# Performance work log

Hardware: AMD Instinct MI355X
Metric: run time of the kernel (lower is better)

## Reference

```python
import jax, jax.numpy as jnp
import numpy as np

B, L, H = 2, 2048, 1024
NH, KVH = 16, 4
HD = H // NH          # 64
G = NH // KVH         # 4 query heads per kv head


def setup_inputs() -> dict:
    key = jax.random.key(0)
    ks = jax.random.split(key, 10)
    s = 0.02
    return {
        "hidden_states": jax.random.normal(ks[0], (B, L, H), dtype=jnp.float32),
        "attention_mask": jnp.zeros((B, 1, L, L), dtype=jnp.float32),
        "Wq": jax.random.normal(ks[1], (H, H), dtype=jnp.float32) * s,
        "bq": jnp.zeros((H,), dtype=jnp.float32),
        "Wk": jax.random.normal(ks[2], (KVH * HD, H), dtype=jnp.float32) * s,
        "bk": jnp.zeros((KVH * HD,), dtype=jnp.float32),
        "Wv": jax.random.normal(ks[3], (KVH * HD, H), dtype=jnp.float32) * s,
        "bv": jnp.zeros((KVH * HD,), dtype=jnp.float32),
        "Wo": jax.random.normal(ks[4], (H, H), dtype=jnp.float32) * s,
        "bo": jnp.zeros((H,), dtype=jnp.float32),
    }


def reference(hidden_states, attention_mask, Wq, bq, Wk, bk, Wv, bv, Wo, bo):
    x = hidden_states
    # projections (torch Linear: x @ W.T + b)
    q = (x @ Wq.T + bq).reshape(B, L, NH, HD).transpose(0, 2, 1, 3)   # [B,NH,L,HD]
    k = (x @ Wk.T + bk).reshape(B, L, KVH, HD).transpose(0, 2, 1, 3)  # [B,KVH,L,HD]
    v = (x @ Wv.T + bv).reshape(B, L, KVH, HD).transpose(0, 2, 1, 3)
    # GQA: group query heads per kv head instead of repeat_interleave (same math)
    qg = q.reshape(B, KVH, G, L, HD)
    scores = jnp.einsum("bkgqd,bkld->bkgql", qg, k) / jnp.sqrt(jnp.float32(HD))
    scores = scores + attention_mask[:, :, None, :, :]  # mask broadcasts over heads
    attn = jax.nn.softmax(scores, axis=-1)              # dropout p=0 -> identity
    ctx = jnp.einsum("bkgql,bkld->bkgqd", attn, v)      # [B,KVH,G,L,HD]
    ctx = ctx.reshape(B, NH, L, HD).transpose(0, 2, 1, 3).reshape(B, L, H)
    return ctx @ Wo.T + bo
```

## Files before the change

### kernel.cpp

```cpp
#include <hip/hip_runtime.h>

#define B_   2
#define L_   2048
#define H_   1024
#define NH_  16
#define KVH_ 4
#define HD_  64

typedef short short8 __attribute__((ext_vector_type(8)));
typedef float f32x4 __attribute__((ext_vector_type(4)));
typedef unsigned short u16x4 __attribute__((ext_vector_type(4)));
typedef unsigned int u32x2 __attribute__((ext_vector_type(2)));

#define LOG2E 1.4426950408889634f
#define QSC   0.18033688011112042f
#define MFMA  __builtin_amdgcn_mfma_f32_16x16x32_bf16

#if __has_builtin(__builtin_amdgcn_exp2f)
#define EXP2(x) __builtin_amdgcn_exp2f(x)
#else
#define EXP2(x) exp2f(x)
#endif

static __device__ __forceinline__ unsigned short f2bf(float f) {
  unsigned int u = __float_as_uint(f);
  u += 0x7FFFu + ((u >> 16) & 1u);
  return (unsigned short)(u >> 16);
}

static __device__ __forceinline__ unsigned int cvtpk(float lo, float hi) {
  unsigned int r;
  asm("v_cvt_pk_bf16_f32 %0, %1, %2" : "=v"(r) : "v"(lo), "v"(hi));
  return r;
}

static __device__ __forceinline__ void gload_lds16(const void* g, void* l) {
  __builtin_amdgcn_global_load_lds(
      (const __attribute__((address_space(1))) unsigned int*)g,
      (__attribute__((address_space(3))) unsigned int*)l, 16, 0, 0);
}

__global__ __launch_bounds__(256) void k_convert_x(const float* __restrict__ x,
                                                   unsigned short* __restrict__ xb) {
  size_t i = ((size_t)blockIdx.x * 256 + threadIdx.x) * 4;
  float4 v = *(const float4*)(x + i);
  u16x4 o = { f2bf(v.x), f2bf(v.y), f2bf(v.z), f2bf(v.w) };
  *(u16x4*)(xb + i) = o;
}

__global__ __launch_bounds__(256) void k_convert_w(const float* __restrict__ Wq,
                                                   const float* __restrict__ Wk,
                                                   const float* __restrict__ Wv,
                                                   const float* __restrict__ Wo,
                                                   unsigned short* __restrict__ wcat,
                                                   unsigned short* __restrict__ wo_b) {
  int r = blockIdx.x;
  int c = threadIdx.x * 4;
  const float* src;
  unsigned short* dst;
  if (r < 1024)      { src = Wq + (size_t)r * 1024;          dst = wcat + (size_t)r * 1024; }
  else if (r < 1280) { src = Wk + (size_t)(r - 1024) * 1024; dst = wcat + (size_t)r * 1024; }
  else if (r < 1536) { src = Wv + (size_t)(r - 1280) * 1024; dst = wcat + (size_t)r * 1024; }
  else               { src = Wo + (size_t)(r - 1536) * 1024; dst = wo_b + (size_t)(r - 1536) * 1024; }
  float4 v = *(const float4*)(src + c);
  u16x4 o = { f2bf(v.x), f2bf(v.y), f2bf(v.z), f2bf(v.w) };
  *(u16x4*)(dst + c) = o;
}

__global__ __launch_bounds__(256) void k_mask_scan(const float* __restrict__ mask,
                                                   unsigned char* __restrict__ flags) {
  const int blk = blockIdx.x;
  const int b = blk >> 10, qb = (blk >> 5) & 31, kb = blk & 31;
  const float* base = mask + ((size_t)b * L_ + qb * 64) * L_ + kb * 64;
  const int t = threadIdx.x;
  const int r0 = t >> 4, c = (t & 15) * 4;
  bool nz = false;
#pragma unroll
  for (int i = 0; i < 4; ++i) {
    float4 v = *(const float4*)(base + (size_t)(r0 + i * 16) * L_ + c);
    nz |= (v.x != 0.f) | (v.y != 0.f) | (v.z != 0.f) | (v.w != 0.f);
  }
  __shared__ int anyv;
  if (t == 0) anyv = 0;
  __syncthreads();
  if (__any(nz) && (t & 63) == 0) atomicOr(&anyv, 1);
  __syncthreads();
  if (t == 0) flags[blk] = (unsigned char)anyv;
}

template <int MODE>
__global__ __launch_bounds__(256) void k_gemm(const unsigned short* __restrict__ A,
                                              const unsigned short* __restrict__ Bt,
                                              const float* __restrict__ bias0,
                                              const float* __restrict__ bias1,
                                              const float* __restrict__ bias2,
                                              unsigned short* __restrict__ q_ws,
                                              unsigned short* __restrict__ k_ws,
                                              unsigned short* __restrict__ vt_ws,
                                              float* __restrict__ outp) {
  const int bn = blockIdx.x, bm = blockIdx.y;
  const int t = threadIdx.x;
  const int lane = t & 63, li = lane & 15, g = lane >> 4;
  const int wid = t >> 6, wr = wid >> 1, wc = wid & 1;
  __shared__ unsigned short lds_a[128 * 32];
  __shared__ unsigned short lds_b[128 * 32];

  const f32x4 z = {0.f, 0.f, 0.f, 0.f};
  f32x4 acc[4][4];
#pragma unroll
  for (int m = 0; m < 4; ++m)
#pragma unroll
    for (int n = 0; n < 4; ++n) acc[m][n] = z;

  const int c0 = t, c1 = 256 + t;
  const int r0 = c0 >> 2, o0 = (c0 & 3) * 8;
  const int r1 = c1 >> 2, o1 = (c1 & 3) * 8;
  const unsigned short* a0p = A + (size_t)(bm * 128 + r0) * 1024 + o0;
  const unsigned short* a1p = A + (size_t)(bm * 128 + r1) * 1024 + o1;
  const unsigned short* b0p = Bt + (size_t)(bn * 128 + r0) * 1024 + o0;
  const unsigned short* b1p = Bt + (size_t)(bn * 128 + r1) * 1024 + o1;

  for (int kt = 0; kt < 1024; kt += 32) {
    gload_lds16(a0p + kt, &lds_a[c0 * 8]);
    gload_lds16(a1p + kt, &lds_a[c1 * 8]);
    gload_lds16(b0p + kt, &lds_b[c0 * 8]);
    gload_lds16(b1p + kt, &lds_b[c1 * 8]);
    __syncthreads();
    short8 af[4], bf[4];
#pragma unroll
    for (int m = 0; m < 4; ++m) af[m] = *(const short8*)&lds_a[(wr * 64 + m * 16 + li) * 32 + g * 8];
#pragma unroll
    for (int n = 0; n < 4; ++n) bf[n] = *(const short8*)&lds_b[(wc * 64 + n * 16 + li) * 32 + g * 8];
#pragma unroll
    for (int m = 0; m < 4; ++m)
#pragma unroll
      for (int n = 0; n < 4; ++n)
        acc[m][n] = MFMA(af[m], bf[n], acc[m][n], 0, 0, 0);
    __syncthreads();
  }

#pragma unroll
  for (int m = 0; m < 4; ++m) {
    const int row0 = bm * 128 + wr * 64 + m * 16 + 4 * g;
#pragma unroll
    for (int n = 0; n < 4; ++n) {
      const int col = bn * 128 + wc * 64 + n * 16 + li;
      f32x4 v = acc[m][n];
      if (MODE == 1) {
        const float bias = bias0[col];
#pragma unroll
        for (int r = 0; r < 4; ++r) outp[(size_t)(row0 + r) * 1024 + col] = v[r] + bias;
      } else {
        if (col < 1024) {
          const float bias = bias0[col];
#pragma unroll
          for (int r = 0; r < 4; ++r) q_ws[(size_t)(row0 + r) * 1024 + col] = f2bf((v[r] + bias) * QSC);
        } else if (col < 1280) {
          const int cc = col - 1024;
          const float bias = bias1[cc];
#pragma unroll
          for (int r = 0; r < 4; ++r) k_ws[(size_t)(row0 + r) * 256 + cc] = f2bf(v[r] + bias);
        } else {
          const int cc = col - 1280;
          const float bias = bias2[cc];
          const int kvh = cc >> 6, d = cc & 63;
          const int b = row0 >> 11, l0 = row0 & 2047;
          u16x4 pk = { f2bf(v[0] + bias), f2bf(v[1] + bias), f2bf(v[2] + bias), f2bf(v[3] + bias) };
          *(u16x4*)(vt_ws + ((size_t)((b * KVH_ + kvh) * 64 + d)) * 2048 + l0) = pk;
        }
      }
    }
  }
}

__global__ __launch_bounds__(256, 2) void k_attn(const unsigned short* __restrict__ q_ws,
                                                 const unsigned short* __restrict__ k_ws,
                                                 const unsigned short* __restrict__ vt_ws,
                                                 const float* __restrict__ mask,
                                                 const unsigned char* __restrict__ mflags,
                                                 unsigned short* __restrict__ ctx) {
  const int bk = blockIdx.x;
  const int qt = blockIdx.y;
  const int b = bk >> 2, kvh = bk & 3;
  const int t = threadIdx.x;
  const int wid = t >> 6, lane = t & 63, li = lane & 15, g = lane >> 4;
  const int h = kvh * 4 + wid;

  __shared__ unsigned short lds_k[2][64 * 64];
  __shared__ unsigned short lds_v[2][64 * 64];
  __shared__ unsigned short lds_p[4][2][16 * 72];

  const unsigned short* qlane = q_ws + ((size_t)b * L_ + qt * 32 + li) * H_ + h * HD_ + g * 8;
  short8 qf[2][2];
#pragma unroll
  for (int qif = 0; qif < 2; ++qif)
#pragma unroll
    for (int hh = 0; hh < 2; ++hh)
      qf[qif][hh] = *(const short8*)(qlane + (size_t)qif * 16 * H_ + hh * 32);

  const unsigned int* fp = (const unsigned int*)(mflags + b * 1024 + (qt >> 1) * 32);
  unsigned int fm = 0;
#pragma unroll
  for (int w = 0; w < 8; ++w) {
    unsigned int wv = fp[w];
    fm |= ((wv & 0x000000FFu) ? 1u : 0u) << (w * 4 + 0);
    fm |= ((wv & 0x0000FF00u) ? 1u : 0u) << (w * 4 + 1);
    fm |= ((wv & 0x00FF0000u) ? 1u : 0u) << (w * 4 + 2);
    fm |= ((wv & 0xFF000000u) ? 1u : 0u) << (w * 4 + 3);
  }
  fm = __builtin_amdgcn_readfirstlane(fm);

  const int srow = t >> 3, sgr = t & 7;
  const int swz = (sgr ^ (srow & 7)) * 8;
  const unsigned short* ksrc = k_ws + ((size_t)b * L_ + srow) * 256 + kvh * 64 + swz;
  const unsigned short* vsrc = vt_ws + ((size_t)(b * KVH_ + kvh) * 64 + srow) * 2048 + swz;

  const f32x4 z = {0.f, 0.f, 0.f, 0.f};
  f32x4 o[2][4];
#pragma unroll
  for (int qif = 0; qif < 2; ++qif)
#pragma unroll
    for (int db = 0; db < 4; ++db) o[qif][db] = z;
  float l_run[2] = {0.f, 0.f};

  const int rsw = li & 7;

#define STAGE(buf, kt)                                                       \
  {                                                                          \
    _Pragma("unroll")                                                        \
    for (int i = 0; i < 2; ++i) {                                            \
      gload_lds16(ksrc + ((size_t)(kt) * 64 + i * 32) * 256,                 \
                  &lds_k[buf][(t + 256 * i) * 8]);                           \
      gload_lds16(vsrc + (size_t)i * 32 * 2048 + (kt) * 64,                  \
                  &lds_v[buf][(t + 256 * i) * 8]);                           \
    }                                                                        \
  }

  STAGE(0, 0);
  __syncthreads();

#pragma unroll 1
  for (int kt = 0; kt < 32; ++kt) {
    const int cur = kt & 1;
    if (kt + 1 < 32) STAGE(cur ^ 1, kt + 1);

    short8 kf[4][2], vf[4][2];
#pragma unroll
    for (int x = 0; x < 4; ++x) {
      const int row = (x * 16 + li) * 64;
      kf[x][0] = *(const short8*)&lds_k[cur][row + ((0 + g) ^ rsw) * 8];
      kf[x][1] = *(const short8*)&lds_k[cur][row + ((4 + g) ^ rsw) * 8];
      vf[x][0] = *(const short8*)&lds_v[cur][row + ((0 + g) ^ rsw) * 8];
      vf[x][1] = *(const short8*)&lds_v[cur][row + ((4 + g) ^ rsw) * 8];
    }

    f32x4 sv[2][4];
    __builtin_amdgcn_s_setprio(1);
#pragma unroll
    for (int qif = 0; qif < 2; ++qif)
#pragma unroll
      for (int kb = 0; kb < 4; ++kb) {
        sv[qif][kb] = MFMA(kf[kb][0], qf[qif][0], z, 0, 0, 0);
        sv[qif][kb] = MFMA(kf[kb][1], qf[qif][1], sv[qif][kb], 0, 0, 0);
      }
    __builtin_amdgcn_s_setprio(0);

    if (fm & (1u << kt)) {
#pragma unroll
      for (int qif = 0; qif < 2; ++qif) {
        const float* mrow = mask + ((size_t)b * L_ + qt * 32 + qif * 16 + li) * L_ + kt * 64 + 4 * g;
#pragma unroll
        for (int kb = 0; kb < 4; ++kb) {
          float4 mv = *(const float4*)(mrow + kb * 16);
          sv[qif][kb][0] = fmaf(mv.x, LOG2E, sv[qif][kb][0]);
          sv[qif][kb][1] = fmaf(mv.y, LOG2E, sv[qif][kb][1]);
          sv[qif][kb][2] = fmaf(mv.z, LOG2E, sv[qif][kb][2]);
          sv[qif][kb][3] = fmaf(mv.w, LOG2E, sv[qif][kb][3]);
        }
      }
    }

#pragma unroll
    for (int qif = 0; qif < 2; ++qif) {
      float ts = 0.f;
#pragma unroll
      for (int kb = 0; kb < 4; ++kb)
#pragma unroll
        for (int r = 0; r < 4; ++r) {
          const float p = EXP2(sv[qif][kb][r]);
          sv[qif][kb][r] = p;
          ts += p;
        }
      l_run[qif] += ts;
#pragma unroll
      for (int kb = 0; kb < 4; ++kb) {
        u32x2 pk = { cvtpk(sv[qif][kb][0], sv[qif][kb][1]),
                     cvtpk(sv[qif][kb][2], sv[qif][kb][3]) };
        *(u32x2*)&lds_p[wid][qif][li * 72 + kb * 16 + 4 * g] = pk;
      }
    }

    __builtin_amdgcn_s_setprio(1);
#pragma unroll
    for (int qif = 0; qif < 2; ++qif)
#pragma unroll
      for (int kjh = 0; kjh < 2; ++kjh) {
        short8 pb = *(const short8*)&lds_p[wid][qif][li * 72 + kjh * 32 + g * 8];
#pragma unroll
        for (int db = 0; db < 4; ++db)
          o[qif][db] = MFMA(vf[db][kjh], pb, o[qif][db], 0, 0, 0);
      }
    __builtin_amdgcn_s_setprio(0);

    __syncthreads();
  }
#undef STAGE

#pragma unroll
  for (int qif = 0; qif < 2; ++qif) {
    float lt = l_run[qif];
    lt += __shfl_xor(lt, 16);
    lt += __shfl_xor(lt, 32);
    const float inv = 1.0f / lt;
    unsigned short* cp = ctx + ((size_t)b * L_ + qt * 32 + qif * 16 + li) * H_ + h * HD_ + 4 * g;
#pragma unroll
    for (int db = 0; db < 4; ++db) {
      u32x2 pk = { cvtpk(o[qif][db][0] * inv, o[qif][db][1] * inv),
                   cvtpk(o[qif][db][2] * inv, o[qif][db][3] * inv) };
      *(u32x2*)(cp + db * 16) = pk;
    }
  }
}

extern "C" void kernel_launch(void* const* d_in, const int* in_sizes, int n_in,
                              void* d_out, int out_size, void* d_ws, size_t ws_size,
                              hipStream_t stream) {
  const float* x    = (const float*)d_in[0];
  const float* mask = (const float*)d_in[1];
  const float* Wq   = (const float*)d_in[2];
  const float* bq   = (const float*)d_in[3];
  const float* Wk   = (const float*)d_in[4];
  const float* bk   = (const float*)d_in[5];
  const float* Wv   = (const float*)d_in[6];
  const float* bv   = (const float*)d_in[7];
  const float* Wo   = (const float*)d_in[8];
  const float* bo   = (const float*)d_in[9];
  float* out = (float*)d_out;

  char* ws = (char*)d_ws;
  unsigned short* xb    = (unsigned short*)(ws);
  unsigned short* ctx   = xb;
  unsigned short* wcat  = (unsigned short*)(ws + 8388608);
  unsigned short* wo_b  = (unsigned short*)(ws + 11534336);
  unsigned short* q_ws  = (unsigned short*)(ws + 13631488);
  unsigned short* k_ws  = (unsigned short*)(ws + 22020096);
  unsigned short* vt_ws = (unsigned short*)(ws + 24117248);
  unsigned char*  mflg  = (unsigned char*)(ws + 26214400);

  k_convert_x<<<dim3(4096), dim3(256), 0, stream>>>(x, xb);
  k_convert_w<<<dim3(2560), dim3(256), 0, stream>>>(Wq, Wk, Wv, Wo, wcat, wo_b);
  k_mask_scan<<<dim3(2048), dim3(256), 0, stream>>>(mask, mflg);
  k_gemm<0><<<dim3(12, 32), dim3(256), 0, stream>>>(xb, wcat, bq, bk, bv, q_ws, k_ws, vt_ws, nullptr);
  k_attn<<<dim3(8, 64), dim3(256), 0, stream>>>(q_ws, k_ws, vt_ws, mask, mflg, ctx);
  k_gemm<1><<<dim3(8, 32), dim3(256), 0, stream>>>(ctx, wo_b, bo, nullptr, nullptr,
                                                   nullptr, nullptr, nullptr, out);
}
```

Measured before the change: 122.0 us.

## Fuse prep kernels and triple-buffer K/V with K-fragment register prefetch

Merges the x conversion, weight conversion and mask scan into one launch, cutting two kernel launches. In attention, K/V LDS staging goes from double to triple buffering with a prefetch distance of two tiles. The next tile's K fragments are read into registers while the current tile's softmax and PV run, with the loop unrolled by two to ping-pong the fragment arrays. This raises LDS use and register pressure, which could lower occupancy at 2 blocks per CU.

```diff
diff --git a/kernel.cpp b/kernel.cpp
--- a/kernel.cpp
+++ b/kernel.cpp
@@ -40,52 +40,53 @@
       (__attribute__((address_space(3))) unsigned int*)l, 16, 0, 0);
 }
 
-__global__ __launch_bounds__(256) void k_convert_x(const float* __restrict__ x,
-                                                   unsigned short* __restrict__ xb) {
-  size_t i = ((size_t)blockIdx.x * 256 + threadIdx.x) * 4;
-  float4 v = *(const float4*)(x + i);
-  u16x4 o = { f2bf(v.x), f2bf(v.y), f2bf(v.z), f2bf(v.w) };
-  *(u16x4*)(xb + i) = o;
-}
-
-__global__ __launch_bounds__(256) void k_convert_w(const float* __restrict__ Wq,
-                                                   const float* __restrict__ Wk,
-                                                   const float* __restrict__ Wv,
-                                                   const float* __restrict__ Wo,
-                                                   unsigned short* __restrict__ wcat,
-                                                   unsigned short* __restrict__ wo_b) {
-  int r = blockIdx.x;
-  int c = threadIdx.x * 4;
-  const float* src;
-  unsigned short* dst;
-  if (r < 1024)      { src = Wq + (size_t)r * 1024;          dst = wcat + (size_t)r * 1024; }
-  else if (r < 1280) { src = Wk + (size_t)(r - 1024) * 1024; dst = wcat + (size_t)r * 1024; }
-  else if (r < 1536) { src = Wv + (size_t)(r - 1280) * 1024; dst = wcat + (size_t)r * 1024; }
-  else               { src = Wo + (size_t)(r - 1536) * 1024; dst = wo_b + (size_t)(r - 1536) * 1024; }
-  float4 v = *(const float4*)(src + c);
-  u16x4 o = { f2bf(v.x), f2bf(v.y), f2bf(v.z), f2bf(v.w) };
-  *(u16x4*)(dst + c) = o;
-}
-
-__global__ __launch_bounds__(256) void k_mask_scan(const float* __restrict__ mask,
-                                                   unsigned char* __restrict__ flags) {
+__global__ __launch_bounds__(256) void k_prep(const float* __restrict__ x,
+                                              const float* __restrict__ Wq,
+                                              const float* __restrict__ Wk,
+                                              const float* __restrict__ Wv,
+                                              const float* __restrict__ Wo,
+                                              const float* __restrict__ mask,
+                                              unsigned short* __restrict__ xb,
+                                              unsigned short* __restrict__ wcat,
+                                              unsigned short* __restrict__ wo_b,
+                                              unsigned char* __restrict__ flags) {
   const int blk = blockIdx.x;
-  const int b = blk >> 10, qb = (blk >> 5) & 31, kb = blk & 31;
-  const float* base = mask + ((size_t)b * L_ + qb * 64) * L_ + kb * 64;
   const int t = threadIdx.x;
-  const int r0 = t >> 4, c = (t & 15) * 4;
-  bool nz = false;
-#pragma unroll
-  for (int i = 0; i < 4; ++i) {
-    float4 v = *(const float4*)(base + (size_t)(r0 + i * 16) * L_ + c);
-    nz |= (v.x != 0.f) | (v.y != 0.f) | (v.z != 0.f) | (v.w != 0.f);
-  }
-  __shared__ int anyv;
-  if (t == 0) anyv = 0;
-  __syncthreads();
-  if (__any(nz) && (t & 63) == 0) atomicOr(&anyv, 1);
-  __syncthreads();
-  if (t == 0) flags[blk] = (unsigned char)anyv;
+  if (blk < 4096) {
+    size_t i = ((size_t)blk * 256 + t) * 4;
+    float4 v = *(const float4*)(x + i);
+    u16x4 o = { f2bf(v.x), f2bf(v.y), f2bf(v.z), f2bf(v.w) };
+    *(u16x4*)(xb + i) = o;
+  } else if (blk < 6656) {
+    int r = blk - 4096;
+    int c = t * 4;
+    const float* src;
+    unsigned short* dst;
+    if (r < 1024)      { src = Wq + (size_t)r * 1024;          dst = wcat + (size_t)r * 1024; }
+    else if (r < 1280) { src = Wk + (size_t)(r - 1024) * 1024; dst = wcat + (size_t)r * 1024; }
+    else if (r < 1536) { src = Wv + (size_t)(r - 1280) * 1024; dst = wcat + (size_t)r * 1024; }
+    else               { src = Wo + (size_t)(r - 1536) * 1024; dst = wo_b + (size_t)(r - 1536) * 1024; }
+    float4 v = *(const float4*)(src + c);
+    u16x4 o = { f2bf(v.x), f2bf(v.y), f2bf(v.z), f2bf(v.w) };
+    *(u16x4*)(dst + c) = o;
+  } else {
+    const int mb = blk - 6656;
+    const int b = mb >> 10, qb = (mb >> 5) & 31, kb = mb & 31;
+    const float* base = mask + ((size_t)b * L_ + qb * 64) * L_ + kb * 64;
+    const int r0 = t >> 4, c = (t & 15) * 4;
+    bool nz = false;
+#pragma unroll
+    for (int i = 0; i < 4; ++i) {
+      float4 v = *(const float4*)(base + (size_t)(r0 + i * 16) * L_ + c);
+      nz |= (v.x != 0.f) | (v.y != 0.f) | (v.z != 0.f) | (v.w != 0.f);
+    }
+    __shared__ int anyv;
+    if (t == 0) anyv = 0;
+    __syncthreads();
+    if (__any(nz) && (t & 63) == 0) atomicOr(&anyv, 1);
+    __syncthreads();
+    if (t == 0) flags[mb] = (unsigned char)anyv;
+  }
 }
 
 template <int MODE>
@@ -186,8 +187,8 @@
   const int wid = t >> 6, lane = t & 63, li = lane & 15, g = lane >> 4;
   const int h = kvh * 4 + wid;
 
-  __shared__ unsigned short lds_k[2][64 * 64];
-  __shared__ unsigned short lds_v[2][64 * 64];
+  __shared__ unsigned short lds_k[3][64 * 64];
+  __shared__ unsigned short lds_v[3][64 * 64];
   __shared__ unsigned short lds_p[4][2][16 * 72];
 
   const unsigned short* qlane = q_ws + ((size_t)b * L_ + qt * 32 + li) * H_ + h * HD_ + g * 8;
@@ -236,20 +237,23 @@
     }                                                                        \
   }
 
-  STAGE(0, 0);
-  __syncthreads();
-
-#pragma unroll 1
-  for (int kt = 0; kt < 32; ++kt) {
-    const int cur = kt & 1;
-    if (kt + 1 < 32) STAGE(cur ^ 1, kt + 1);
-
-    short8 kf[4][2], vf[4][2];
+  auto readK = [&](short8 (&kf)[4][2], int buf) {
 #pragma unroll
     for (int x = 0; x < 4; ++x) {
       const int row = (x * 16 + li) * 64;
-      kf[x][0] = *(const short8*)&lds_k[cur][row + ((0 + g) ^ rsw) * 8];
-      kf[x][1] = *(const short8*)&lds_k[cur][row + ((4 + g) ^ rsw) * 8];
+      kf[x][0] = *(const short8*)&lds_k[buf][row + ((0 + g) ^ rsw) * 8];
+      kf[x][1] = *(const short8*)&lds_k[buf][row + ((4 + g) ^ rsw) * 8];
+    }
+  };
+
+  auto tile = [&](short8 (&kfc)[4][2], short8 (&kfn)[4][2], int kt) {
+    const int cur = kt % 3;
+    if (kt + 2 < 32) STAGE((kt + 2) % 3, kt + 2);
+
+    short8 vf[4][2];
+#pragma unroll
+    for (int x = 0; x < 4; ++x) {
+      const int row = (x * 16 + li) * 64;
       vf[x][0] = *(const short8*)&lds_v[cur][row + ((0 + g) ^ rsw) * 8];
       vf[x][1] = *(const short8*)&lds_v[cur][row + ((4 + g) ^ rsw) * 8];
     }
@@ -260,10 +264,12 @@
     for (int qif = 0; qif < 2; ++qif)
 #pragma unroll
       for (int kb = 0; kb < 4; ++kb) {
-        sv[qif][kb] = MFMA(kf[kb][0], qf[qif][0], z, 0, 0, 0);
-        sv[qif][kb] = MFMA(kf[kb][1], qf[qif][1], sv[qif][kb], 0, 0, 0);
+        sv[qif][kb] = MFMA(kfc[kb][0], qf[qif][0], z, 0, 0, 0);
+        sv[qif][kb] = MFMA(kfc[kb][1], qf[qif][1], sv[qif][kb], 0, 0, 0);
       }
     __builtin_amdgcn_s_setprio(0);
+
+    if (kt + 1 < 32) readK(kfn, (kt + 1) % 3);
 
     if (fm & (1u << kt)) {
 #pragma unroll
@@ -313,6 +319,20 @@
     __builtin_amdgcn_s_setprio(0);
 
     __syncthreads();
+  };
+
+  STAGE(0, 0);
+  __syncthreads();
+  STAGE(1, 1);
+  __syncthreads();
+
+  short8 kfA[4][2], kfB[4][2];
+  readK(kfA, 0);
+
+#pragma unroll 1
+  for (int kt = 0; kt < 32; kt += 2) {
+    tile(kfA, kfB, kt);
+    tile(kfB, kfA, kt + 1);
   }
 #undef STAGE
 
@@ -357,9 +377,7 @@
   unsigned short* vt_ws = (unsigned short*)(ws + 24117248);
   unsigned char*  mflg  = (unsigned char*)(ws + 26214400);
 
-  k_convert_x<<<dim3(4096), dim3(256), 0, stream>>>(x, xb);
-  k_convert_w<<<dim3(2560), dim3(256), 0, stream>>>(Wq, Wk, Wv, Wo, wcat, wo_b);
-  k_mask_scan<<<dim3(2048), dim3(256), 0, stream>>>(mask, mflg);
+  k_prep<<<dim3(8704), dim3(256), 0, stream>>>(x, Wq, Wk, Wv, Wo, mask, xb, wcat, wo_b, mflg);
   k_gemm<0><<<dim3(12, 32), dim3(256), 0, stream>>>(xb, wcat, bq, bk, bv, q_ws, k_ws, vt_ws, nullptr);
   k_attn<<<dim3(8, 64), dim3(256), 0, stream>>>(q_ws, k_ws, vt_ws, mask, mflg, ctx);
   k_gemm<1><<<dim3(8, 32), dim3(256), 0, stream>>>(ctx, wo_b, bo, nullptr, nullptr,
```

New measurement: 116.5 us. -4.5%, faster.
